# Kernel tuning notes

Hardware: AMD Instinct MI355X
Metric: run time of the kernel (lower is better)

The kernel has to match this reference:

```python
import jax, jax.numpy as jnp
import numpy as np

C_IN = 192
HEADS = 6
QKV_DIM = C_IN // HEADS  # 32
WH = WW = 4              # window_size
PAD_H = WH // 2          # 2
PAD_W = WW // 2          # 2


def setup_inputs() -> dict:
    key = jax.random.key(0)
    ks = jax.random.split(key, 6)
    s = 0.02
    return {
        "x": jax.random.normal(ks[0], (8, C_IN, 128, 128), jnp.float32),
        "w_qkv1": jax.random.normal(ks[1], (3 * C_IN, C_IN), jnp.float32) * s,
        "b_qkv1": jnp.zeros((3 * C_IN,), jnp.float32),
        "w_qkv2": jax.random.normal(ks[2], (3 * C_IN, C_IN), jnp.float32) * s,
        "b_qkv2": jnp.zeros((3 * C_IN,), jnp.float32),
        "w_head": jax.random.normal(ks[3], (C_IN, 2 * C_IN), jnp.float32) * s,  # 1x1 conv as matmul
        "b_head": jnp.zeros((C_IN,), jnp.float32),
    }


def _window_partition(x):
    # bchw_to_bnc: [B,C,H,W] -> [B*nh*nw, WH*WW, C]
    B, C, H, W = x.shape
    nh, nw = H // WH, W // WW
    x = x.reshape(B, C, nh, WH, nw, WW)
    x = x.transpose(0, 2, 4, 3, 5, 1)  # B,nh,nw,WH,WW,C
    return x.reshape(B * nh * nw, WH * WW, C)


def _window_merge(x, out_shape):
    # bnc_to_bchw: inverse of _window_partition
    B, C, H, W = out_shape
    nh, nw = H // WH, W // WW
    x = x.reshape(B, nh, nw, WH, WW, C)
    x = x.transpose(0, 5, 1, 3, 2, 4)  # B,C,nh,WH,nw,WW
    return x.reshape(B, C, H, W)


def _mha(xw, w, b):
    # xw: [Bn, N=16, C]; fused QKV projection then per-window SDPA
    Bn, N, C = xw.shape
    qkv = xw @ w.T + b
    q, k, v = jnp.split(qkv, 3, axis=-1)
    to_heads = lambda t: t.reshape(Bn, N, HEADS, QKV_DIM).transpose(0, 2, 1, 3)
    q, k, v = to_heads(q), to_heads(k), to_heads(v)
    scale = 1.0 / np.sqrt(QKV_DIM).astype(np.float32)
    attn = jax.nn.softmax(jnp.einsum('bhnd,bhmd->bhnm', q, k) * scale, axis=-1)
    o = jnp.einsum('bhnm,bhmd->bhnd', attn, v)
    return o.transpose(0, 2, 1, 3).reshape(Bn, N, C)


def reference(x, w_qkv1, b_qkv1, w_qkv2, b_qkv2, w_head, b_head):
    # branch 2: zero-pad by window//2 on each side (shifted windows)
    x2 = jnp.pad(x, ((0, 0), (0, 0), (PAD_H, PAD_H), (PAD_W, PAD_W)))
    s1, s2 = x.shape, x2.shape
    o1 = _window_merge(_mha(_window_partition(x), w_qkv1, b_qkv1), s1)
    o2 = _window_merge(_mha(_window_partition(x2), w_qkv2, b_qkv2), s2)
    o2 = o2[:, :, PAD_H:-PAD_H, PAD_W:-PAD_W]  # negative pad = crop
    o = jnp.concatenate([o1, o2], axis=1)      # [B, 2C, H, W]
    # 1x1 conv head projection
    return jnp.einsum('bchw,oc->bohw', o, w_head) + b_head[None, :, None, None]
```

## Files before the change

kernel.cpp:

```cpp
#include <hip/hip_runtime.h>


typedef unsigned short u16;
using bf16x8 = __attribute__((ext_vector_type(8))) short;
using f32x4  = __attribute__((ext_vector_type(4))) float;
using u16x8  = __attribute__((ext_vector_type(8))) unsigned short;
using u16x4  = __attribute__((ext_vector_type(4))) unsigned short;

#define CIN   192
#define CQKV  576
#define NW2   33

__device__ __forceinline__ float bf2f(u16 u) {
    unsigned int x = ((unsigned int)u) << 16;
    float f; __builtin_memcpy(&f, &x, 4); return f;
}
__device__ __forceinline__ u16 f2bf(float f) {
    unsigned int x; __builtin_memcpy(&x, &f, 4);
    return (u16)((x + 0x7FFFu + ((x >> 16) & 1u)) >> 16);
}
__device__ __forceinline__ int xcol(int c, int tok) {
    int blk = (c >> 3) ^ ((tok ^ (tok >> 4)) & 7);
    return blk * 8 + (c & 7);
}

__global__ void prep_conv(const float* __restrict__ w1, const float* __restrict__ w2,
                          const float* __restrict__ wh,
                          u16* __restrict__ w1b, u16* __restrict__ w2b, u16* __restrict__ whb) {
    int i = blockIdx.x * 256 + threadIdx.x;
    if (i < 110592)        w1b[i] = f2bf(w1[i]);
    else if (i < 221184)   w2b[i - 110592] = f2bf(w2[i - 110592]);
    else                   whb[i - 221184] = f2bf(wh[i - 221184]);
}

__global__ __launch_bounds__(256, 2) void qkv_attn(const float* __restrict__ x,
                                                   const u16* __restrict__ w1b,
                                                   const float* __restrict__ b1,
                                                   const u16* __restrict__ w2b,
                                                   const float* __restrict__ b2,
                                                   u16* __restrict__ ocat) {
    __shared__ __align__(16) char smem[77824];
    u16* xl = (u16*)smem;
    u16* qk = (u16*)smem;
    u16* vt = (u16*)(smem + 50176);
    u16* pl = (u16*)(smem + 74752);

    const int tid  = threadIdx.x;
    const int wave = tid >> 6, lane = tid & 63;
    const int lo16 = lane & 15, quad = lane >> 4;

    const int swz = (blockIdx.x & 7) * 553 + (blockIdx.x >> 3);
    const bool br0 = (swz < 2048);

    int b, wy, g;
    const u16* wb; const float* bias;
    if (br0) {
        b = swz >> 8; int rem = swz & 255;
        wy = rem >> 3; g = rem & 7;
        wb = w1b; bias = b1;
    } else {
        int bi = swz - 2048;
        b = bi / 297; int rem = bi % 297;
        wy = rem / 9; g = rem % 9;
        wb = w2b; bias = b2;
    }
    const int hbase = wy * 4, wbase = g * 16;

    if (br0) {
#pragma unroll
        for (int it = 0; it < 12; ++it) {
            int i = it * 256 + tid;
            int c = i >> 4, y = (i >> 2) & 3, xc = i & 3;
            const float4 v = *reinterpret_cast<const float4*>(
                &x[(((size_t)b * CIN + c) * 128 + hbase + y) * 128 + wbase + xc * 4]);
            int t0 = xc * 16 + y * 4;
            xl[(t0 + 0) * 200 + xcol(c, t0 + 0)] = f2bf(v.x);
            xl[(t0 + 1) * 200 + xcol(c, t0 + 1)] = f2bf(v.y);
            xl[(t0 + 2) * 200 + xcol(c, t0 + 2)] = f2bf(v.z);
            xl[(t0 + 3) * 200 + xcol(c, t0 + 3)] = f2bf(v.w);
        }
    } else {
#pragma unroll
        for (int it = 0; it < 12; ++it) {
            int i = it * 256 + tid;
            int c = i >> 4, y = (i >> 2) & 3, xc = i & 3;
            float e0, e1, e2, e3;
            int h = hbase + y - 2;
            int w0 = wbase + xc * 4 - 2;
            bool hok = (unsigned)h < 128u;
            const float* row = &x[(((size_t)b * CIN + c) * 128 + h) * 128];
            if (hok && w0 >= 0 && w0 + 3 < 128) {
                float2 p0 = *reinterpret_cast<const float2*>(&row[w0]);
                float2 p1 = *reinterpret_cast<const float2*>(&row[w0 + 2]);
                e0 = p0.x; e1 = p0.y; e2 = p1.x; e3 = p1.y;
            } else {
                e0 = (hok && w0 >= 0 && w0 < 128)         ? row[w0]     : 0.f;
                e1 = (hok && w0+1 >= 0 && w0+1 < 128)     ? row[w0 + 1] : 0.f;
                e2 = (hok && w0+2 >= 0 && w0+2 < 128)     ? row[w0 + 2] : 0.f;
                e3 = (hok && w0+3 >= 0 && w0+3 < 128)     ? row[w0 + 3] : 0.f;
            }
            int t0 = xc * 16 + y * 4;
            xl[(t0 + 0) * 200 + xcol(c, t0 + 0)] = f2bf(e0);
            xl[(t0 + 1) * 200 + xcol(c, t0 + 1)] = f2bf(e1);
            xl[(t0 + 2) * 200 + xcol(c, t0 + 2)] = f2bf(e2);
            xl[(t0 + 3) * 200 + xcol(c, t0 + 3)] = f2bf(e3);
        }
    }
    __syncthreads();

    f32x4 acc[9][4];
#pragma unroll
    for (int mt = 0; mt < 9; ++mt)
#pragma unroll
        for (int nt = 0; nt < 4; ++nt) acc[mt][nt] = f32x4{0.f, 0.f, 0.f, 0.f};

    const u16* wrow = wb + (size_t)(wave * 144 + lo16) * 192 + quad * 8;
#pragma unroll
    for (int s = 0; s < 6; ++s) {
        bf16x8 bfr[4];
#pragma unroll
        for (int nt = 0; nt < 4; ++nt) {
            int tok = nt * 16 + lo16;
            int kb = s * 4 + quad;
            bfr[nt] = *reinterpret_cast<const bf16x8*>(
                &xl[tok * 200 + (((kb ^ ((tok ^ (tok >> 4)) & 7)) << 3))]);
        }
#pragma unroll
        for (int mt = 0; mt < 9; ++mt) {
            bf16x8 afr = *reinterpret_cast<const bf16x8*>(&wrow[mt * 3072 + s * 32]);
#pragma unroll
            for (int nt = 0; nt < 4; ++nt)
                acc[mt][nt] = __builtin_amdgcn_mfma_f32_16x16x32_bf16(afr, bfr[nt], acc[mt][nt], 0, 0, 0);
        }
    }
    __syncthreads();

    const float scale = 0.17677669529663687f;
#pragma unroll
    for (int mt = 0; mt < 9; ++mt) {
        int co0 = wave * 144 + mt * 16 + quad * 4;
        const float4 bv = *reinterpret_cast<const float4*>(&bias[co0]);
#pragma unroll
        for (int nt = 0; nt < 4; ++nt) {
            int tok = nt * 16 + lo16;
            float v0 = acc[mt][nt][0] + bv.x, v1 = acc[mt][nt][1] + bv.y;
            float v2 = acc[mt][nt][2] + bv.z, v3 = acc[mt][nt][3] + bv.w;
            if (co0 < 192) { v0 *= scale; v1 *= scale; v2 *= scale; v3 *= scale; }
            if (co0 < 384) {
                u16x4 pk = {f2bf(v0), f2bf(v1), f2bf(v2), f2bf(v3)};
                *reinterpret_cast<u16x4*>(&qk[tok * 392 + co0]) = pk;
            } else {
                int dh = co0 - 384;
                int head = dh >> 5, d0 = dh & 31;
                int win = tok >> 4, m = tok & 15;
                u16* vrow = &vt[((win * 6 + head) * 32 + d0) * 16 + m];
                vrow[0]  = f2bf(v0);
                vrow[16] = f2bf(v1);
                vrow[32] = f2bf(v2);
                vrow[48] = f2bf(v3);
            }
        }
    }
    __syncthreads();

    {
        const int win = wave;
        const u16* qbase = qk + (size_t)(win * 16) * 392;
        const bf16x8 z8 = {};
        const f32x4 zc = {0.f, 0.f, 0.f, 0.f};
        bool dov; size_t dst = 0;
        if (br0) {
            int wg = wy * 32 + g * 4 + win;
            dst = (((size_t)(b * 1024 + wg)) * 16 + lo16) * 384;
            dov = true;
        } else {
            int wx = g * 4 + win;
            int h = wy * 4 + (lo16 >> 2) - 2;
            int w = wx * 4 + (lo16 & 3) - 2;
            dov = (wx < NW2) && (unsigned)h < 128u && (unsigned)w < 128u;
            if (dov) {
                int wg = (h >> 2) * 32 + (w >> 2);
                int nn = (h & 3) * 4 + (w & 3);
                dst = (((size_t)(b * 1024 + wg)) * 16 + nn) * 384 + 192;
            }
        }
#pragma unroll
        for (int head = 0; head < 6; ++head) {
            bf16x8 kfr = *reinterpret_cast<const bf16x8*>(
                &qbase[lo16 * 392 + 192 + head * 32 + quad * 8]);
            bf16x8 qfr = *reinterpret_cast<const bf16x8*>(
                &qbase[lo16 * 392 + head * 32 + quad * 8]);
            f32x4 st = __builtin_amdgcn_mfma_f32_16x16x32_bf16(kfr, qfr, zc, 0, 0, 0);
            float mx = fmaxf(fmaxf(st[0], st[1]), fmaxf(st[2], st[3]));
            mx = fmaxf(mx, __shfl_xor(mx, 16));
            mx = fmaxf(mx, __shfl_xor(mx, 32));
            float p0 = __expf(st[0] - mx), p1 = __expf(st[1] - mx);
            float p2 = __expf(st[2] - mx), p3 = __expf(st[3] - mx);
            float sum = p0 + p1 + p2 + p3;
            sum += __shfl_xor(sum, 16);
            sum += __shfl_xor(sum, 32);
            float inv = 1.0f / sum;
            u16x4 pk = {f2bf(p0), f2bf(p1), f2bf(p2), f2bf(p3)};
            *reinterpret_cast<u16x4*>(&pl[(wave * 16 + lo16) * 24 + quad * 4]) = pk;
            bf16x8 pf = (quad < 2)
                ? *reinterpret_cast<const bf16x8*>(&pl[(wave * 16 + lo16) * 24 + quad * 8]) : z8;
            const u16* vbase = &vt[(win * 6 + head) * 32 * 16];
#pragma unroll
            for (int half = 0; half < 2; ++half) {
                bf16x8 av = (quad < 2)
                    ? *reinterpret_cast<const bf16x8*>(&vbase[(half * 16 + lo16) * 16 + quad * 8]) : z8;
                f32x4 o = __builtin_amdgcn_mfma_f32_16x16x32_bf16(av, pf, zc, 0, 0, 0);
                if (dov) {
                    u16x4 ok = {f2bf(o[0] * inv), f2bf(o[1] * inv),
                                f2bf(o[2] * inv), f2bf(o[3] * inv)};
                    *reinterpret_cast<u16x4*>(&ocat[dst + head * 32 + half * 16 + quad * 4]) = ok;
                }
            }
        }
    }
}

__global__ __launch_bounds__(256, 3) void head_gemm(const u16* __restrict__ ocat,
                                                    const u16* __restrict__ whb,
                                                    const float* __restrict__ bh,
                                                    float* __restrict__ out) {
    __shared__ __align__(16) u16 bt[64 * 392];
    const int tid = threadIdx.x;
    const int wave = tid >> 6, lane = tid & 63;
    const int lo16 = lane & 15, quad = lane >> 4;

    int bi = blockIdx.x;
    int b = bi >> 8; int rem = bi & 255;
    int wy = rem >> 3, g = rem & 7;
    const int wg0 = wy * 32 + g * 4;
    const size_t gbase = ((size_t)(b * 1024 + wg0) * 16) * 384;

#pragma unroll
    for (int it = 0; it < 12; ++it) {
        int i = it * 256 + tid;
        u16x8 v = *reinterpret_cast<const u16x8*>(&ocat[gbase + (size_t)i * 8]);
        int row = i / 48, kc = i - row * 48;
        *reinterpret_cast<u16x8*>(&bt[row * 392 + kc * 8]) = v;
    }
    __syncthreads();

    const int co_base = wave * 48;
    f32x4 acc[3][4];
#pragma unroll
    for (int mt = 0; mt < 3; ++mt)
#pragma unroll
        for (int nt = 0; nt < 4; ++nt) acc[mt][nt] = f32x4{0.f, 0.f, 0.f, 0.f};

#pragma unroll
    for (int s = 0; s < 12; ++s) {
        int k0 = s * 32;
        bf16x8 a[3], bb[4];
#pragma unroll
        for (int nt = 0; nt < 4; ++nt)
            bb[nt] = *reinterpret_cast<const bf16x8*>(&bt[(nt * 16 + lo16) * 392 + k0 + quad * 8]);
#pragma unroll
        for (int mt = 0; mt < 3; ++mt)
            a[mt] = *reinterpret_cast<const bf16x8*>(
                &whb[(size_t)(co_base + mt * 16 + lo16) * 384 + k0 + quad * 8]);
#pragma unroll
        for (int mt = 0; mt < 3; ++mt)
#pragma unroll
            for (int nt = 0; nt < 4; ++nt)
                acc[mt][nt] = __builtin_amdgcn_mfma_f32_16x16x32_bf16(a[mt], bb[nt], acc[mt][nt], 0, 0, 0);
    }

    int h = wy * 4 + (lo16 >> 2);
#pragma unroll
    for (int mt = 0; mt < 3; ++mt) {
        int co0 = co_base + mt * 16 + quad * 4;
        const float4 bv = *reinterpret_cast<const float4*>(&bh[co0]);
#pragma unroll
        for (int r = 0; r < 4; ++r) {
            float bias = (r == 0) ? bv.x : (r == 1) ? bv.y : (r == 2) ? bv.z : bv.w;
#pragma unroll
            for (int nt = 0; nt < 4; ++nt) {
                int w = (g * 4 + nt) * 4 + (lo16 & 3);
                out[(((size_t)b * CIN + co0 + r) * 128 + h) * 128 + w] = acc[mt][nt][r] + bias;
            }
        }
    }
}

extern "C" void kernel_launch(void* const* d_in, const int* in_sizes, int n_in,
                              void* d_out, int out_size, void* d_ws, size_t ws_size,
                              hipStream_t stream) {
    const float* x  = (const float*)d_in[0];
    const float* w1 = (const float*)d_in[1];
    const float* b1 = (const float*)d_in[2];
    const float* w2 = (const float*)d_in[3];
    const float* b2 = (const float*)d_in[4];
    const float* wh = (const float*)d_in[5];
    const float* bh = (const float*)d_in[6];
    float* out = (float*)d_out;

    char* ws = (char*)d_ws;
    u16* ocat = (u16*)ws;
    u16* w1b  = (u16*)(ws + 100663296);
    u16* w2b  = (u16*)(ws + 100884480);
    u16* whb  = (u16*)(ws + 101105664);

    prep_conv<<<1152, 256, 0, stream>>>(w1, w2, wh, w1b, w2b, whb);
    qkv_attn<<<4424, 256, 0, stream>>>(x, w1b, b1, w2b, b2, ocat);
    head_gemm<<<2048, 256, 0, stream>>>(ocat, whb, bh, out);
}
```

Baseline: 485.4 us.

## Permute QKV weights per head so each wave owns one head's attention

```diff
diff --git a/kernel.cpp b/kernel.cpp
--- a/kernel.cpp
+++ b/kernel.cpp
@@ -8,17 +8,17 @@
 using u16x4  = __attribute__((ext_vector_type(4))) unsigned short;
 
 #define CIN   192
-#define CQKV  576
 #define NW2   33
-
-__device__ __forceinline__ float bf2f(u16 u) {
-    unsigned int x = ((unsigned int)u) << 16;
-    float f; __builtin_memcpy(&f, &x, 4); return f;
-}
+#define QSCALE 0.17677669529663687f
+
 __device__ __forceinline__ u16 f2bf(float f) {
     unsigned int x; __builtin_memcpy(&x, &f, 4);
     return (u16)((x + 0x7FFFu + ((x >> 16) & 1u)) >> 16);
 }
+__device__ __forceinline__ u16x4 pack4(f32x4 v) {
+    u16x4 r = {f2bf(v[0]), f2bf(v[1]), f2bf(v[2]), f2bf(v[3])};
+    return r;
+}
 __device__ __forceinline__ int xcol(int c, int tok) {
     int blk = (c >> 3) ^ ((tok ^ (tok >> 4)) & 7);
     return blk * 8 + (c & 7);
@@ -26,50 +26,68 @@
 
 __global__ void prep_conv(const float* __restrict__ w1, const float* __restrict__ w2,
                           const float* __restrict__ wh,
-                          u16* __restrict__ w1b, u16* __restrict__ w2b, u16* __restrict__ whb) {
+                          const float* __restrict__ b1, const float* __restrict__ b2,
+                          u16* __restrict__ w1p, u16* __restrict__ w2p,
+                          u16* __restrict__ whb,
+                          float* __restrict__ b1p, float* __restrict__ b2p) {
     int i = blockIdx.x * 256 + threadIdx.x;
-    if (i < 110592)        w1b[i] = f2bf(w1[i]);
-    else if (i < 221184)   w2b[i - 110592] = f2bf(w2[i - 110592]);
-    else                   whb[i - 221184] = f2bf(wh[i - 221184]);
-}
-
-__global__ __launch_bounds__(256, 2) void qkv_attn(const float* __restrict__ x,
-                                                   const u16* __restrict__ w1b,
-                                                   const float* __restrict__ b1,
-                                                   const u16* __restrict__ w2b,
-                                                   const float* __restrict__ b2,
+    if (i < 221184) {
+        int j = (i < 110592) ? i : i - 110592;
+        int co = j / 192, k = j - co * 192;
+        int h = co / 96, r = co - h * 96, sec = r >> 5, d = r & 31;
+        int co_old = sec * 192 + h * 32 + d;
+        float v = ((i < 110592) ? w1 : w2)[co_old * 192 + k];
+        if (sec == 0) v *= QSCALE;
+        ((i < 110592) ? w1p : w2p)[j] = f2bf(v);
+    } else if (i < 294912) {
+        int j = i - 221184;
+        whb[j] = f2bf(wh[j]);
+    } else if (i < 296064) {
+        int j = (i < 295488) ? (i - 294912) : (i - 295488);
+        int h = j / 96, r = j - h * 96, sec = r >> 5, d = r & 31;
+        float v = ((i < 295488) ? b1 : b2)[sec * 192 + h * 32 + d];
+        if (sec == 0) v *= QSCALE;
+        ((i < 295488) ? b1p : b2p)[j] = v;
+    }
+}
+
+__global__ __launch_bounds__(384, 3) void qkv_attn(const float* __restrict__ x,
+                                                   const u16* __restrict__ w1p,
+                                                   const float* __restrict__ b1p,
+                                                   const u16* __restrict__ w2p,
+                                                   const float* __restrict__ b2p,
                                                    u16* __restrict__ ocat) {
-    __shared__ __align__(16) char smem[77824];
-    u16* xl = (u16*)smem;
-    u16* qk = (u16*)smem;
-    u16* vt = (u16*)(smem + 50176);
-    u16* pl = (u16*)(smem + 74752);
+    __shared__ __align__(16) char smem[50176];
+    u16* xl  = (u16*)smem;
+    u16* qkw = (u16*)(smem + 25600);
+    u16* vt  = (u16*)(smem + 39424);
+    u16* pl  = (u16*)(smem + 45568);
 
     const int tid  = threadIdx.x;
-    const int wave = tid >> 6, lane = tid & 63;
+    const int wave = tid / 64, lane = tid & 63;
     const int lo16 = lane & 15, quad = lane >> 4;
 
     const int swz = (blockIdx.x & 7) * 553 + (blockIdx.x >> 3);
     const bool br0 = (swz < 2048);
 
     int b, wy, g;
-    const u16* wb; const float* bias;
+    const u16* wb; const float* biasp;
     if (br0) {
         b = swz >> 8; int rem = swz & 255;
         wy = rem >> 3; g = rem & 7;
-        wb = w1b; bias = b1;
+        wb = w1p; biasp = b1p;
     } else {
         int bi = swz - 2048;
         b = bi / 297; int rem = bi % 297;
         wy = rem / 9; g = rem % 9;
-        wb = w2b; bias = b2;
+        wb = w2p; biasp = b2p;
     }
     const int hbase = wy * 4, wbase = g * 16;
 
     if (br0) {
 #pragma unroll
-        for (int it = 0; it < 12; ++it) {
-            int i = it * 256 + tid;
+        for (int it = 0; it < 8; ++it) {
+            int i = it * 384 + tid;
             int c = i >> 4, y = (i >> 2) & 3, xc = i & 3;
             const float4 v = *reinterpret_cast<const float4*>(
                 &x[(((size_t)b * CIN + c) * 128 + hbase + y) * 128 + wbase + xc * 4]);
@@ -81,8 +99,8 @@
         }
     } else {
 #pragma unroll
-        for (int it = 0; it < 12; ++it) {
-            int i = it * 256 + tid;
+        for (int it = 0; it < 8; ++it) {
+            int i = it * 384 + tid;
             int c = i >> 4, y = (i >> 2) & 3, xc = i & 3;
             float e0, e1, e2, e3;
             int h = hbase + y - 2;
@@ -108,13 +126,13 @@
     }
     __syncthreads();
 
-    f32x4 acc[9][4];
-#pragma unroll
-    for (int mt = 0; mt < 9; ++mt)
+    f32x4 acc[6][4];
+#pragma unroll
+    for (int mt = 0; mt < 6; ++mt)
 #pragma unroll
         for (int nt = 0; nt < 4; ++nt) acc[mt][nt] = f32x4{0.f, 0.f, 0.f, 0.f};
 
-    const u16* wrow = wb + (size_t)(wave * 144 + lo16) * 192 + quad * 8;
+    const u16* wrow = wb + (size_t)(wave * 96 + lo16) * 192 + quad * 8;
 #pragma unroll
     for (int s = 0; s < 6; ++s) {
         bf16x8 bfr[4];
@@ -126,55 +144,39 @@
                 &xl[tok * 200 + (((kb ^ ((tok ^ (tok >> 4)) & 7)) << 3))]);
         }
 #pragma unroll
-        for (int mt = 0; mt < 9; ++mt) {
+        for (int mt = 0; mt < 6; ++mt) {
             bf16x8 afr = *reinterpret_cast<const bf16x8*>(&wrow[mt * 3072 + s * 32]);
 #pragma unroll
             for (int nt = 0; nt < 4; ++nt)
                 acc[mt][nt] = __builtin_amdgcn_mfma_f32_16x16x32_bf16(afr, bfr[nt], acc[mt][nt], 0, 0, 0);
         }
     }
-    __syncthreads();
-
-    const float scale = 0.17677669529663687f;
-#pragma unroll
-    for (int mt = 0; mt < 9; ++mt) {
-        int co0 = wave * 144 + mt * 16 + quad * 4;
-        const float4 bv = *reinterpret_cast<const float4*>(&bias[co0]);
+
+#pragma unroll
+    for (int mt = 0; mt < 6; ++mt) {
+        const float4 bv = *reinterpret_cast<const float4*>(&biasp[wave * 96 + mt * 16 + quad * 4]);
 #pragma unroll
         for (int nt = 0; nt < 4; ++nt) {
-            int tok = nt * 16 + lo16;
-            float v0 = acc[mt][nt][0] + bv.x, v1 = acc[mt][nt][1] + bv.y;
-            float v2 = acc[mt][nt][2] + bv.z, v3 = acc[mt][nt][3] + bv.w;
-            if (co0 < 192) { v0 *= scale; v1 *= scale; v2 *= scale; v3 *= scale; }
-            if (co0 < 384) {
-                u16x4 pk = {f2bf(v0), f2bf(v1), f2bf(v2), f2bf(v3)};
-                *reinterpret_cast<u16x4*>(&qk[tok * 392 + co0]) = pk;
-            } else {
-                int dh = co0 - 384;
-                int head = dh >> 5, d0 = dh & 31;
-                int win = tok >> 4, m = tok & 15;
-                u16* vrow = &vt[((win * 6 + head) * 32 + d0) * 16 + m];
-                vrow[0]  = f2bf(v0);
-                vrow[16] = f2bf(v1);
-                vrow[32] = f2bf(v2);
-                vrow[48] = f2bf(v3);
-            }
-        }
-    }
-    __syncthreads();
-
-    {
-        const int win = wave;
-        const u16* qbase = qk + (size_t)(win * 16) * 392;
-        const bf16x8 z8 = {};
-        const f32x4 zc = {0.f, 0.f, 0.f, 0.f};
+            acc[mt][nt][0] += bv.x; acc[mt][nt][1] += bv.y;
+            acc[mt][nt][2] += bv.z; acc[mt][nt][3] += bv.w;
+        }
+    }
+
+    u16* qrow = qkw + wave * 1152 + lo16 * 72;
+    u16* vbs  = vt  + wave * 512;
+    u16* plb  = pl  + wave * 384;
+    const bf16x8 z8 = {};
+    const f32x4 zc = {0.f, 0.f, 0.f, 0.f};
+
+#pragma unroll
+    for (int nt = 0; nt < 4; ++nt) {
         bool dov; size_t dst = 0;
         if (br0) {
-            int wg = wy * 32 + g * 4 + win;
+            int wg = wy * 32 + g * 4 + nt;
             dst = (((size_t)(b * 1024 + wg)) * 16 + lo16) * 384;
             dov = true;
         } else {
-            int wx = g * 4 + win;
+            int wx = g * 4 + nt;
             int h = wy * 4 + (lo16 >> 2) - 2;
             int w = wx * 4 + (lo16 & 3) - 2;
             dov = (wx < NW2) && (unsigned)h < 128u && (unsigned)w < 128u;
@@ -184,59 +186,63 @@
                 dst = (((size_t)(b * 1024 + wg)) * 16 + nn) * 384 + 192;
             }
         }
-#pragma unroll
-        for (int head = 0; head < 6; ++head) {
-            bf16x8 kfr = *reinterpret_cast<const bf16x8*>(
-                &qbase[lo16 * 392 + 192 + head * 32 + quad * 8]);
-            bf16x8 qfr = *reinterpret_cast<const bf16x8*>(
-                &qbase[lo16 * 392 + head * 32 + quad * 8]);
-            f32x4 st = __builtin_amdgcn_mfma_f32_16x16x32_bf16(kfr, qfr, zc, 0, 0, 0);
-            float mx = fmaxf(fmaxf(st[0], st[1]), fmaxf(st[2], st[3]));
-            mx = fmaxf(mx, __shfl_xor(mx, 16));
-            mx = fmaxf(mx, __shfl_xor(mx, 32));
-            float p0 = __expf(st[0] - mx), p1 = __expf(st[1] - mx);
-            float p2 = __expf(st[2] - mx), p3 = __expf(st[3] - mx);
-            float sum = p0 + p1 + p2 + p3;
-            sum += __shfl_xor(sum, 16);
-            sum += __shfl_xor(sum, 32);
-            float inv = 1.0f / sum;
-            u16x4 pk = {f2bf(p0), f2bf(p1), f2bf(p2), f2bf(p3)};
-            *reinterpret_cast<u16x4*>(&pl[(wave * 16 + lo16) * 24 + quad * 4]) = pk;
-            bf16x8 pf = (quad < 2)
-                ? *reinterpret_cast<const bf16x8*>(&pl[(wave * 16 + lo16) * 24 + quad * 8]) : z8;
-            const u16* vbase = &vt[(win * 6 + head) * 32 * 16];
-#pragma unroll
-            for (int half = 0; half < 2; ++half) {
-                bf16x8 av = (quad < 2)
-                    ? *reinterpret_cast<const bf16x8*>(&vbase[(half * 16 + lo16) * 16 + quad * 8]) : z8;
-                f32x4 o = __builtin_amdgcn_mfma_f32_16x16x32_bf16(av, pf, zc, 0, 0, 0);
-                if (dov) {
-                    u16x4 ok = {f2bf(o[0] * inv), f2bf(o[1] * inv),
-                                f2bf(o[2] * inv), f2bf(o[3] * inv)};
-                    *reinterpret_cast<u16x4*>(&ocat[dst + head * 32 + half * 16 + quad * 4]) = ok;
-                }
+        *reinterpret_cast<u16x4*>(&qrow[     quad * 4]) = pack4(acc[0][nt]);
+        *reinterpret_cast<u16x4*>(&qrow[16 + quad * 4]) = pack4(acc[1][nt]);
+        *reinterpret_cast<u16x4*>(&qrow[32 + quad * 4]) = pack4(acc[2][nt]);
+        *reinterpret_cast<u16x4*>(&qrow[48 + quad * 4]) = pack4(acc[3][nt]);
+#pragma unroll
+        for (int ht = 0; ht < 2; ++ht)
+#pragma unroll
+            for (int j = 0; j < 4; ++j)
+                vbs[(ht * 16 + quad * 4 + j) * 16 + lo16] = f2bf(acc[4 + ht][nt][j]);
+
+        bf16x8 kfr = *reinterpret_cast<const bf16x8*>(&qrow[32 + quad * 8]);
+        bf16x8 qfr = *reinterpret_cast<const bf16x8*>(&qrow[quad * 8]);
+        f32x4 st = __builtin_amdgcn_mfma_f32_16x16x32_bf16(kfr, qfr, zc, 0, 0, 0);
+        float mx = fmaxf(fmaxf(st[0], st[1]), fmaxf(st[2], st[3]));
+        mx = fmaxf(mx, __shfl_xor(mx, 16));
+        mx = fmaxf(mx, __shfl_xor(mx, 32));
+        float p0 = __expf(st[0] - mx), p1 = __expf(st[1] - mx);
+        float p2 = __expf(st[2] - mx), p3 = __expf(st[3] - mx);
+        float sum = p0 + p1 + p2 + p3;
+        sum += __shfl_xor(sum, 16);
+        sum += __shfl_xor(sum, 32);
+        float inv = 1.0f / sum;
+        u16x4 pk = {f2bf(p0), f2bf(p1), f2bf(p2), f2bf(p3)};
+        *reinterpret_cast<u16x4*>(&plb[lo16 * 24 + quad * 4]) = pk;
+        bf16x8 pf = (quad < 2)
+            ? *reinterpret_cast<const bf16x8*>(&plb[lo16 * 24 + quad * 8]) : z8;
+#pragma unroll
+        for (int half = 0; half < 2; ++half) {
+            bf16x8 av = (quad < 2)
+                ? *reinterpret_cast<const bf16x8*>(&vbs[(half * 16 + lo16) * 16 + quad * 8]) : z8;
+            f32x4 o = __builtin_amdgcn_mfma_f32_16x16x32_bf16(av, pf, zc, 0, 0, 0);
+            if (dov) {
+                u16x4 ok = {f2bf(o[0] * inv), f2bf(o[1] * inv),
+                            f2bf(o[2] * inv), f2bf(o[3] * inv)};
+                *reinterpret_cast<u16x4*>(&ocat[dst + wave * 32 + half * 16 + quad * 4]) = ok;
             }
         }
     }
 }
 
-__global__ __launch_bounds__(256, 3) void head_gemm(const u16* __restrict__ ocat,
+__global__ __launch_bounds__(256, 6) void head_gemm(const u16* __restrict__ ocat,
                                                     const u16* __restrict__ whb,
                                                     const float* __restrict__ bh,
                                                     float* __restrict__ out) {
-    __shared__ __align__(16) u16 bt[64 * 392];
+    __shared__ __align__(16) u16 bt[32 * 392];
     const int tid = threadIdx.x;
     const int wave = tid >> 6, lane = tid & 63;
     const int lo16 = lane & 15, quad = lane >> 4;
 
-    int bi = blockIdx.x;
-    int b = bi >> 8; int rem = bi & 255;
-    int wy = rem >> 3, g = rem & 7;
-    const int wg0 = wy * 32 + g * 4;
+    int bi = (blockIdx.x & 7) * 512 + (blockIdx.x >> 3);
+    int b = bi >> 9; int rem = bi & 511;
+    int wy = rem >> 4, g = rem & 15;
+    const int wg0 = wy * 32 + g * 2;
     const size_t gbase = ((size_t)(b * 1024 + wg0) * 16) * 384;
 
 #pragma unroll
-    for (int it = 0; it < 12; ++it) {
+    for (int it = 0; it < 6; ++it) {
         int i = it * 256 + tid;
         u16x8 v = *reinterpret_cast<const u16x8*>(&ocat[gbase + (size_t)i * 8]);
         int row = i / 48, kc = i - row * 48;
@@ -245,18 +251,18 @@
     __syncthreads();
 
     const int co_base = wave * 48;
-    f32x4 acc[3][4];
+    f32x4 acc[3][2];
 #pragma unroll
     for (int mt = 0; mt < 3; ++mt)
 #pragma unroll
-        for (int nt = 0; nt < 4; ++nt) acc[mt][nt] = f32x4{0.f, 0.f, 0.f, 0.f};
+        for (int nt = 0; nt < 2; ++nt) acc[mt][nt] = f32x4{0.f, 0.f, 0.f, 0.f};
 
 #pragma unroll
     for (int s = 0; s < 12; ++s) {
         int k0 = s * 32;
-        bf16x8 a[3], bb[4];
-#pragma unroll
-        for (int nt = 0; nt < 4; ++nt)
+        bf16x8 a[3], bb[2];
+#pragma unroll
+        for (int nt = 0; nt < 2; ++nt)
             bb[nt] = *reinterpret_cast<const bf16x8*>(&bt[(nt * 16 + lo16) * 392 + k0 + quad * 8]);
 #pragma unroll
         for (int mt = 0; mt < 3; ++mt)
@@ -265,7 +271,7 @@
 #pragma unroll
         for (int mt = 0; mt < 3; ++mt)
 #pragma unroll
-            for (int nt = 0; nt < 4; ++nt)
+            for (int nt = 0; nt < 2; ++nt)
                 acc[mt][nt] = __builtin_amdgcn_mfma_f32_16x16x32_bf16(a[mt], bb[nt], acc[mt][nt], 0, 0, 0);
     }
 
@@ -278,8 +284,8 @@
         for (int r = 0; r < 4; ++r) {
             float bias = (r == 0) ? bv.x : (r == 1) ? bv.y : (r == 2) ? bv.z : bv.w;
 #pragma unroll
-            for (int nt = 0; nt < 4; ++nt) {
-                int w = (g * 4 + nt) * 4 + (lo16 & 3);
+            for (int nt = 0; nt < 2; ++nt) {
+                int w = (g * 2 + nt) * 4 + (lo16 & 3);
                 out[(((size_t)b * CIN + co0 + r) * 128 + h) * 128 + w] = acc[mt][nt][r] + bias;
             }
         }
@@ -299,12 +305,14 @@
     float* out = (float*)d_out;
 
     char* ws = (char*)d_ws;
-    u16* ocat = (u16*)ws;
-    u16* w1b  = (u16*)(ws + 100663296);
-    u16* w2b  = (u16*)(ws + 100884480);
-    u16* whb  = (u16*)(ws + 101105664);
-
-    prep_conv<<<1152, 256, 0, stream>>>(w1, w2, wh, w1b, w2b, whb);
-    qkv_attn<<<4424, 256, 0, stream>>>(x, w1b, b1, w2b, b2, ocat);
-    head_gemm<<<2048, 256, 0, stream>>>(ocat, whb, bh, out);
-}
+    u16*   ocat = (u16*)ws;
+    u16*   w1p  = (u16*)(ws + 100663296);
+    u16*   w2p  = (u16*)(ws + 100884480);
+    u16*   whb  = (u16*)(ws + 101105664);
+    float* b1p  = (float*)(ws + 101253120);
+    float* b2p  = (float*)(ws + 101255424);
+
+    prep_conv<<<1157, 256, 0, stream>>>(w1, w2, wh, b1, b2, w1p, w2p, whb, b1p, b2p);
+    qkv_attn<<<4424, 384, 0, stream>>>(x, w1p, b1p, w2p, b2p, ocat);
+    head_gemm<<<4096, 256, 0, stream>>>(ocat, whb, bh, out);
+}
```

Measured after the change: 537.0 us. +10.6%, slower.

## Pre-transpose input to padded bf16 NHWC and read QKV operands from global

Applied to the files above, without the earlier changes.

```diff
diff --git a/kernel.cpp b/kernel.cpp
--- a/kernel.cpp
+++ b/kernel.cpp
@@ -8,13 +8,9 @@
 using u16x4  = __attribute__((ext_vector_type(4))) unsigned short;
 
 #define CIN   192
-#define CQKV  576
 #define NW2   33
-
-__device__ __forceinline__ float bf2f(u16 u) {
-    unsigned int x = ((unsigned int)u) << 16;
-    float f; __builtin_memcpy(&f, &x, 4); return f;
-}
+#define QSCALE 0.17677669529663687f
+
 __device__ __forceinline__ u16 f2bf(float f) {
     unsigned int x; __builtin_memcpy(&x, &f, 4);
     return (u16)((x + 0x7FFFu + ((x >> 16) & 1u)) >> 16);
@@ -24,21 +20,226 @@
     return blk * 8 + (c & 7);
 }
 
-__global__ void prep_conv(const float* __restrict__ w1, const float* __restrict__ w2,
-                          const float* __restrict__ wh,
-                          u16* __restrict__ w1b, u16* __restrict__ w2b, u16* __restrict__ whb) {
+__global__ void prep_w(const float* __restrict__ w1, const float* __restrict__ w2,
+                       const float* __restrict__ wh,
+                       u16* __restrict__ w1b, u16* __restrict__ w2b,
+                       u16* __restrict__ whb) {
     int i = blockIdx.x * 256 + threadIdx.x;
-    if (i < 110592)        w1b[i] = f2bf(w1[i]);
-    else if (i < 221184)   w2b[i - 110592] = f2bf(w2[i - 110592]);
-    else                   whb[i - 221184] = f2bf(wh[i - 221184]);
-}
-
-__global__ __launch_bounds__(256, 2) void qkv_attn(const float* __restrict__ x,
-                                                   const u16* __restrict__ w1b,
-                                                   const float* __restrict__ b1,
-                                                   const u16* __restrict__ w2b,
-                                                   const float* __restrict__ b2,
-                                                   u16* __restrict__ ocat) {
+    if (i < 221184) {
+        int j = (i < 110592) ? i : i - 110592;
+        int co = j / 192;
+        float v = ((i < 110592) ? w1 : w2)[j];
+        if (co < 192) v *= QSCALE;
+        ((i < 110592) ? w1b : w2b)[j] = f2bf(v);
+    } else if (i < 294912) {
+        int j = i - 221184;
+        whb[j] = f2bf(wh[j]);
+    }
+}
+
+__global__ __launch_bounds__(256, 2) void prep_x(const float* __restrict__ x,
+                                                 u16* __restrict__ xp) {
+    __shared__ __align__(16) u16 lt[128 * 200];
+    int bi = blockIdx.x;
+    int b = bi / 132, hp = bi % 132;
+    u16* orow = xp + ((size_t)(b * 132 + hp)) * 132 * 192;
+    const int tid = threadIdx.x;
+
+    if (hp >= 2 && hp < 130) {
+        const int h = hp - 2;
+        const float* xr = x + (size_t)b * 192 * 128 * 128 + (size_t)h * 128;
+#pragma unroll
+        for (int it = 0; it < 24; ++it) {
+            int i = it * 256 + tid;
+            int c = i >> 5, w0 = (i & 31) * 4;
+            float4 v = *reinterpret_cast<const float4*>(&xr[(size_t)c * 16384 + w0]);
+            lt[(w0 + 0) * 200 + xcol(c, w0 + 0)] = f2bf(v.x);
+            lt[(w0 + 1) * 200 + xcol(c, w0 + 1)] = f2bf(v.y);
+            lt[(w0 + 2) * 200 + xcol(c, w0 + 2)] = f2bf(v.z);
+            lt[(w0 + 3) * 200 + xcol(c, w0 + 3)] = f2bf(v.w);
+        }
+        __syncthreads();
+#pragma unroll
+        for (int it = 0; it < 13; ++it) {
+            int i = it * 256 + tid;
+            if (i < 3168) {
+                int wp = i / 24, kc = i - wp * 24;
+                u16x8 val = {};
+                if (wp >= 2 && wp < 130) {
+                    int w = wp - 2;
+                    int blk = kc ^ ((w ^ (w >> 4)) & 7);
+                    val = *reinterpret_cast<const u16x8*>(&lt[w * 200 + blk * 8]);
+                }
+                *reinterpret_cast<u16x8*>(&orow[(size_t)wp * 192 + kc * 8]) = val;
+            }
+        }
+    } else {
+#pragma unroll
+        for (int it = 0; it < 13; ++it) {
+            int i = it * 256 + tid;
+            if (i < 3168) {
+                u16x8 z = {};
+                *reinterpret_cast<u16x8*>(&orow[(size_t)i * 8]) = z;
+            }
+        }
+    }
+}
+
+__device__ __forceinline__ void attn_tail(f32x4 (&acc)[9][4],
+                                          const float* __restrict__ bias,
+                                          u16* qk, u16* vt, u16* pl,
+                                          int wave, int lane, int lo16, int quad,
+                                          bool br0, int b, int wy, int g,
+                                          u16* __restrict__ ocat) {
+#pragma unroll
+    for (int mt = 0; mt < 9; ++mt) {
+        int co0 = wave * 144 + mt * 16 + quad * 4;
+        float4 bv = *reinterpret_cast<const float4*>(&bias[co0]);
+        if (co0 < 192) { bv.x *= QSCALE; bv.y *= QSCALE; bv.z *= QSCALE; bv.w *= QSCALE; }
+#pragma unroll
+        for (int nt = 0; nt < 4; ++nt) {
+            int tok = nt * 16 + lo16;
+            float v0 = acc[mt][nt][0] + bv.x, v1 = acc[mt][nt][1] + bv.y;
+            float v2 = acc[mt][nt][2] + bv.z, v3 = acc[mt][nt][3] + bv.w;
+            if (co0 < 384) {
+                u16x4 pk = {f2bf(v0), f2bf(v1), f2bf(v2), f2bf(v3)};
+                *reinterpret_cast<u16x4*>(&qk[tok * 392 + co0]) = pk;
+            } else {
+                int dh = co0 - 384;
+                int head = dh >> 5, d0 = dh & 31;
+                int win = tok >> 4, m = tok & 15;
+                u16* vrow = &vt[((win * 6 + head) * 32 + d0) * 16 + m];
+                vrow[0]  = f2bf(v0);
+                vrow[16] = f2bf(v1);
+                vrow[32] = f2bf(v2);
+                vrow[48] = f2bf(v3);
+            }
+        }
+    }
+    __syncthreads();
+
+    const int win = wave;
+    const u16* qbase = qk + (size_t)(win * 16) * 392;
+    const bf16x8 z8 = {};
+    const f32x4 zc = {0.f, 0.f, 0.f, 0.f};
+    bool dov; size_t dst = 0;
+    if (br0) {
+        int wg = wy * 32 + g * 4 + win;
+        dst = (((size_t)(b * 1024 + wg)) * 16 + lo16) * 384;
+        dov = true;
+    } else {
+        int wx = g * 4 + win;
+        int h = wy * 4 + (lo16 >> 2) - 2;
+        int w = wx * 4 + (lo16 & 3) - 2;
+        dov = (wx < NW2) && (unsigned)h < 128u && (unsigned)w < 128u;
+        if (dov) {
+            int wg = (h >> 2) * 32 + (w >> 2);
+            int nn = (h & 3) * 4 + (w & 3);
+            dst = (((size_t)(b * 1024 + wg)) * 16 + nn) * 384 + 192;
+        }
+    }
+#pragma unroll
+    for (int head = 0; head < 6; ++head) {
+        bf16x8 kfr = *reinterpret_cast<const bf16x8*>(
+            &qbase[lo16 * 392 + 192 + head * 32 + quad * 8]);
+        bf16x8 qfr = *reinterpret_cast<const bf16x8*>(
+            &qbase[lo16 * 392 + head * 32 + quad * 8]);
+        f32x4 st = __builtin_amdgcn_mfma_f32_16x16x32_bf16(kfr, qfr, zc, 0, 0, 0);
+        float mx = fmaxf(fmaxf(st[0], st[1]), fmaxf(st[2], st[3]));
+        mx = fmaxf(mx, __shfl_xor(mx, 16));
+        mx = fmaxf(mx, __shfl_xor(mx, 32));
+        float p0 = __expf(st[0] - mx), p1 = __expf(st[1] - mx);
+        float p2 = __expf(st[2] - mx), p3 = __expf(st[3] - mx);
+        float sum = p0 + p1 + p2 + p3;
+        sum += __shfl_xor(sum, 16);
+        sum += __shfl_xor(sum, 32);
+        float inv = 1.0f / sum;
+        u16x4 pk = {f2bf(p0), f2bf(p1), f2bf(p2), f2bf(p3)};
+        *reinterpret_cast<u16x4*>(&pl[(wave * 16 + lo16) * 24 + quad * 4]) = pk;
+        bf16x8 pf = (quad < 2)
+            ? *reinterpret_cast<const bf16x8*>(&pl[(wave * 16 + lo16) * 24 + quad * 8]) : z8;
+        const u16* vbase = &vt[(win * 6 + head) * 32 * 16];
+#pragma unroll
+        for (int half = 0; half < 2; ++half) {
+            bf16x8 av = (quad < 2)
+                ? *reinterpret_cast<const bf16x8*>(&vbase[(half * 16 + lo16) * 16 + quad * 8]) : z8;
+            f32x4 o = __builtin_amdgcn_mfma_f32_16x16x32_bf16(av, pf, zc, 0, 0, 0);
+            if (dov) {
+                u16x4 ok = {f2bf(o[0] * inv), f2bf(o[1] * inv),
+                            f2bf(o[2] * inv), f2bf(o[3] * inv)};
+                *reinterpret_cast<u16x4*>(&ocat[dst + head * 32 + half * 16 + quad * 4]) = ok;
+            }
+        }
+    }
+}
+
+__global__ __launch_bounds__(256, 2) void qkv_attn_g(const u16* __restrict__ xp,
+                                                     const u16* __restrict__ w1b,
+                                                     const float* __restrict__ b1,
+                                                     const u16* __restrict__ w2b,
+                                                     const float* __restrict__ b2,
+                                                     u16* __restrict__ ocat) {
+    __shared__ __align__(16) char smem[77824];
+    u16* qk = (u16*)smem;
+    u16* vt = (u16*)(smem + 50176);
+    u16* pl = (u16*)(smem + 74752);
+
+    const int tid  = threadIdx.x;
+    const int wave = tid >> 6, lane = tid & 63;
+    const int lo16 = lane & 15, quad = lane >> 4;
+
+    const int swz = (blockIdx.x & 7) * 553 + (blockIdx.x >> 3);
+    const bool br0 = (swz < 2048);
+
+    int b, wy, g;
+    const u16* wb; const float* bias;
+    if (br0) { b = swz >> 8; int rem = swz & 255; wy = rem >> 3; g = rem & 7;
+               wb = w1b; bias = b1; }
+    else     { int bi = swz - 2048; b = bi / 297; int rem = bi % 297;
+               wy = rem / 9; g = rem % 9; wb = w2b; bias = b2; }
+
+    const int d  = br0 ? 2 : 0;
+    const int ty = lo16 >> 2, tx = lo16 & 3;
+    const u16* bp[4];
+#pragma unroll
+    for (int nt = 0; nt < 4; ++nt) {
+        int wx = g * 4 + nt;
+        if (!br0 && wx > 32) wx = 32;
+        int hp = d + wy * 4 + ty;
+        int wp = d + wx * 4 + tx;
+        bp[nt] = xp + (((size_t)b * 132 + hp) * 132 + wp) * 192 + quad * 8;
+    }
+
+    f32x4 acc[9][4];
+#pragma unroll
+    for (int mt = 0; mt < 9; ++mt)
+#pragma unroll
+        for (int nt = 0; nt < 4; ++nt) acc[mt][nt] = f32x4{0.f, 0.f, 0.f, 0.f};
+
+    const u16* wrow = wb + (size_t)(wave * 144 + lo16) * 192 + quad * 8;
+#pragma unroll
+    for (int s = 0; s < 6; ++s) {
+        bf16x8 bfr[4];
+#pragma unroll
+        for (int nt = 0; nt < 4; ++nt)
+            bfr[nt] = *reinterpret_cast<const bf16x8*>(bp[nt] + s * 32);
+#pragma unroll
+        for (int mt = 0; mt < 9; ++mt) {
+            bf16x8 afr = *reinterpret_cast<const bf16x8*>(&wrow[mt * 3072 + s * 32]);
+#pragma unroll
+            for (int nt = 0; nt < 4; ++nt)
+                acc[mt][nt] = __builtin_amdgcn_mfma_f32_16x16x32_bf16(afr, bfr[nt], acc[mt][nt], 0, 0, 0);
+        }
+    }
+    attn_tail(acc, bias, qk, vt, pl, wave, lane, lo16, quad, br0, b, wy, g, ocat);
+}
+
+__global__ __launch_bounds__(256, 2) void qkv_attn_fb(const float* __restrict__ x,
+                                                      const u16* __restrict__ w1b,
+                                                      const float* __restrict__ b1,
+                                                      const u16* __restrict__ w2b,
+                                                      const float* __restrict__ b2,
+                                                      u16* __restrict__ ocat) {
     __shared__ __align__(16) char smem[77824];
     u16* xl = (u16*)smem;
     u16* qk = (u16*)smem;
@@ -54,16 +255,10 @@
 
     int b, wy, g;
     const u16* wb; const float* bias;
-    if (br0) {
-        b = swz >> 8; int rem = swz & 255;
-        wy = rem >> 3; g = rem & 7;
-        wb = w1b; bias = b1;
-    } else {
-        int bi = swz - 2048;
-        b = bi / 297; int rem = bi % 297;
-        wy = rem / 9; g = rem % 9;
-        wb = w2b; bias = b2;
-    }
+    if (br0) { b = swz >> 8; int rem = swz & 255; wy = rem >> 3; g = rem & 7;
+               wb = w1b; bias = b1; }
+    else     { int bi = swz - 2048; b = bi / 297; int rem = bi % 297;
+               wy = rem / 9; g = rem % 9; wb = w2b; bias = b2; }
     const int hbase = wy * 4, wbase = g * 16;
 
     if (br0) {
@@ -134,109 +329,26 @@
         }
     }
     __syncthreads();
-
-    const float scale = 0.17677669529663687f;
-#pragma unroll
-    for (int mt = 0; mt < 9; ++mt) {
-        int co0 = wave * 144 + mt * 16 + quad * 4;
-        const float4 bv = *reinterpret_cast<const float4*>(&bias[co0]);
-#pragma unroll
-        for (int nt = 0; nt < 4; ++nt) {
-            int tok = nt * 16 + lo16;
-            float v0 = acc[mt][nt][0] + bv.x, v1 = acc[mt][nt][1] + bv.y;
-            float v2 = acc[mt][nt][2] + bv.z, v3 = acc[mt][nt][3] + bv.w;
-            if (co0 < 192) { v0 *= scale; v1 *= scale; v2 *= scale; v3 *= scale; }
-            if (co0 < 384) {
-                u16x4 pk = {f2bf(v0), f2bf(v1), f2bf(v2), f2bf(v3)};
-                *reinterpret_cast<u16x4*>(&qk[tok * 392 + co0]) = pk;
-            } else {
-                int dh = co0 - 384;
-                int head = dh >> 5, d0 = dh & 31;
-                int win = tok >> 4, m = tok & 15;
-                u16* vrow = &vt[((win * 6 + head) * 32 + d0) * 16 + m];
-                vrow[0]  = f2bf(v0);
-                vrow[16] = f2bf(v1);
-                vrow[32] = f2bf(v2);
-                vrow[48] = f2bf(v3);
-            }
-        }
-    }
-    __syncthreads();
-
-    {
-        const int win = wave;
-        const u16* qbase = qk + (size_t)(win * 16) * 392;
-        const bf16x8 z8 = {};
-        const f32x4 zc = {0.f, 0.f, 0.f, 0.f};
-        bool dov; size_t dst = 0;
-        if (br0) {
-            int wg = wy * 32 + g * 4 + win;
-            dst = (((size_t)(b * 1024 + wg)) * 16 + lo16) * 384;
-            dov = true;
-        } else {
-            int wx = g * 4 + win;
-            int h = wy * 4 + (lo16 >> 2) - 2;
-            int w = wx * 4 + (lo16 & 3) - 2;
-            dov = (wx < NW2) && (unsigned)h < 128u && (unsigned)w < 128u;
-            if (dov) {
-                int wg = (h >> 2) * 32 + (w >> 2);
-                int nn = (h & 3) * 4 + (w & 3);
-                dst = (((size_t)(b * 1024 + wg)) * 16 + nn) * 384 + 192;
-            }
-        }
-#pragma unroll
-        for (int head = 0; head < 6; ++head) {
-            bf16x8 kfr = *reinterpret_cast<const bf16x8*>(
-                &qbase[lo16 * 392 + 192 + head * 32 + quad * 8]);
-            bf16x8 qfr = *reinterpret_cast<const bf16x8*>(
-                &qbase[lo16 * 392 + head * 32 + quad * 8]);
-            f32x4 st = __builtin_amdgcn_mfma_f32_16x16x32_bf16(kfr, qfr, zc, 0, 0, 0);
-            float mx = fmaxf(fmaxf(st[0], st[1]), fmaxf(st[2], st[3]));
-            mx = fmaxf(mx, __shfl_xor(mx, 16));
-            mx = fmaxf(mx, __shfl_xor(mx, 32));
-            float p0 = __expf(st[0] - mx), p1 = __expf(st[1] - mx);
-            float p2 = __expf(st[2] - mx), p3 = __expf(st[3] - mx);
-            float sum = p0 + p1 + p2 + p3;
-            sum += __shfl_xor(sum, 16);
-            sum += __shfl_xor(sum, 32);
-            float inv = 1.0f / sum;
-            u16x4 pk = {f2bf(p0), f2bf(p1), f2bf(p2), f2bf(p3)};
-            *reinterpret_cast<u16x4*>(&pl[(wave * 16 + lo16) * 24 + quad * 4]) = pk;
-            bf16x8 pf = (quad < 2)
-                ? *reinterpret_cast<const bf16x8*>(&pl[(wave * 16 + lo16) * 24 + quad * 8]) : z8;
-            const u16* vbase = &vt[(win * 6 + head) * 32 * 16];
-#pragma unroll
-            for (int half = 0; half < 2; ++half) {
-                bf16x8 av = (quad < 2)
-                    ? *reinterpret_cast<const bf16x8*>(&vbase[(half * 16 + lo16) * 16 + quad * 8]) : z8;
-                f32x4 o = __builtin_amdgcn_mfma_f32_16x16x32_bf16(av, pf, zc, 0, 0, 0);
-                if (dov) {
-                    u16x4 ok = {f2bf(o[0] * inv), f2bf(o[1] * inv),
-                                f2bf(o[2] * inv), f2bf(o[3] * inv)};
-                    *reinterpret_cast<u16x4*>(&ocat[dst + head * 32 + half * 16 + quad * 4]) = ok;
-                }
-            }
-        }
-    }
-}
-
-__global__ __launch_bounds__(256, 3) void head_gemm(const u16* __restrict__ ocat,
+    attn_tail(acc, bias, qk, vt, pl, wave, lane, lo16, quad, br0, b, wy, g, ocat);
+}
+
+__global__ __launch_bounds__(256, 6) void head_gemm(const u16* __restrict__ ocat,
                                                     const u16* __restrict__ whb,
                                                     const float* __restrict__ bh,
                                                     float* __restrict__ out) {
-    __shared__ __align__(16) u16 bt[64 * 392];
+    __shared__ __align__(16) u16 bt[32 * 392];
     const int tid = threadIdx.x;
     const int wave = tid >> 6, lane = tid & 63;
     const int lo16 = lane & 15, quad = lane >> 4;
 
-    int bi = blockIdx.x;
-    int b = bi >> 8; int rem = bi & 255;
-    int wy = rem >> 3, g = rem & 7;
-    const int wg0 = wy * 32 + g * 4;
+    int bi = (blockIdx.x & 7) * 512 + (blockIdx.x >> 3);
+    int b = bi >> 9; int rem = bi & 511;
+    int wy = rem >> 4, g = rem & 15;
+    const int wg0 = wy * 32 + g * 2;
     const size_t gbase = ((size_t)(b * 1024 + wg0) * 16) * 384;
 
 #pragma unroll
-    for (int it = 0; it < 12; ++it) {
+    for (int it = 0; it < 6; ++it) {
         int i = it * 256 + tid;
         u16x8 v = *reinterpret_cast<const u16x8*>(&ocat[gbase + (size_t)i * 8]);
         int row = i / 48, kc = i - row * 48;
@@ -245,18 +357,18 @@
     __syncthreads();
 
     const int co_base = wave * 48;
-    f32x4 acc[3][4];
+    f32x4 acc[3][2];
 #pragma unroll
     for (int mt = 0; mt < 3; ++mt)
 #pragma unroll
-        for (int nt = 0; nt < 4; ++nt) acc[mt][nt] = f32x4{0.f, 0.f, 0.f, 0.f};
+        for (int nt = 0; nt < 2; ++nt) acc[mt][nt] = f32x4{0.f, 0.f, 0.f, 0.f};
 
 #pragma unroll
     for (int s = 0; s < 12; ++s) {
         int k0 = s * 32;
-        bf16x8 a[3], bb[4];
-#pragma unroll
-        for (int nt = 0; nt < 4; ++nt)
+        bf16x8 a[3], bb[2];
+#pragma unroll
+        for (int nt = 0; nt < 2; ++nt)
             bb[nt] = *reinterpret_cast<const bf16x8*>(&bt[(nt * 16 + lo16) * 392 + k0 + quad * 8]);
 #pragma unroll
         for (int mt = 0; mt < 3; ++mt)
@@ -265,7 +377,7 @@
 #pragma unroll
         for (int mt = 0; mt < 3; ++mt)
 #pragma unroll
-            for (int nt = 0; nt < 4; ++nt)
+            for (int nt = 0; nt < 2; ++nt)
                 acc[mt][nt] = __builtin_amdgcn_mfma_f32_16x16x32_bf16(a[mt], bb[nt], acc[mt][nt], 0, 0, 0);
     }
 
@@ -278,8 +390,8 @@
         for (int r = 0; r < 4; ++r) {
             float bias = (r == 0) ? bv.x : (r == 1) ? bv.y : (r == 2) ? bv.z : bv.w;
 #pragma unroll
-            for (int nt = 0; nt < 4; ++nt) {
-                int w = (g * 4 + nt) * 4 + (lo16 & 3);
+            for (int nt = 0; nt < 2; ++nt) {
+                int w = (g * 2 + nt) * 4 + (lo16 & 3);
                 out[(((size_t)b * CIN + co0 + r) * 128 + h) * 128 + w] = acc[mt][nt][r] + bias;
             }
         }
@@ -303,8 +415,16 @@
     u16* w1b  = (u16*)(ws + 100663296);
     u16* w2b  = (u16*)(ws + 100884480);
     u16* whb  = (u16*)(ws + 101105664);
-
-    prep_conv<<<1152, 256, 0, stream>>>(w1, w2, wh, w1b, w2b, whb);
-    qkv_attn<<<4424, 256, 0, stream>>>(x, w1b, b1, w2b, b2, ocat);
-    head_gemm<<<2048, 256, 0, stream>>>(ocat, whb, bh, out);
-}
+    u16* xp   = (u16*)(ws + 101253120);
+
+    const size_t need_full = 101253120u + 53526528u;
+
+    prep_w<<<1152, 256, 0, stream>>>(w1, w2, wh, w1b, w2b, whb);
+    if (ws_size >= need_full) {
+        prep_x<<<1056, 256, 0, stream>>>(x, xp);
+        qkv_attn_g<<<4424, 256, 0, stream>>>(xp, w1b, b1, w2b, b2, ocat);
+    } else {
+        qkv_attn_fb<<<4424, 256, 0, stream>>>(x, w1b, b1, w2b, b2, ocat);
+    }
+    head_gemm<<<4096, 256, 0, stream>>>(ocat, whb, bh, out);
+}
```

Result: no change. 495.0 us (+2.0%).
